# Kernel tuning notes

Measured on AMD Instinct MI355X. Metric: run time of the kernel, lower is better.

Reference implementation:

```python
import jax, jax.numpy as jnp
import numpy as np

S, B, H = 4096, 1, 2048       # [seq, batch, hidden] layout (NeoX convention)
NP, HN = 16, H // 16          # heads, head dim
ROT = int(HN * 0.25)          # rotary_ndims = 32 (rotary_pct=0.25)
ROPE_BASE = 10000.0


def setup_inputs() -> dict:
    key = jax.random.key(0)
    k0, k1, k2 = jax.random.split(key, 3)
    hidden_states = jax.random.normal(k0, (S, B, H), jnp.float32) * 0.02
    # causal left-to-right mask: True = masked out (filled with -10000)
    attention_mask = jnp.triu(jnp.ones((1, 1, S, S), bool), k=1)
    w_qkv = jax.random.normal(k1, (3 * H, H), jnp.float32) * (1.0 / np.sqrt(H))
    w_dense = jax.random.normal(k2, (H, H), jnp.float32) * (1.0 / np.sqrt(H))
    b_dense = jnp.zeros((H,), jnp.float32)
    return {"hidden_states": hidden_states, "attention_mask": attention_mask,
            "w_qkv": w_qkv, "w_dense": w_dense, "b_dense": b_dense}


def _apply_rope(x, pos):
    # x: [s, b, np, ROT]; NeoX rotate_half convention
    inv_freq = 1.0 / (ROPE_BASE ** (jnp.arange(0, ROT, 2, dtype=jnp.float32) / ROT))
    freqs = pos[:, None] * inv_freq[None, :]              # [s, ROT/2]
    emb = jnp.concatenate([freqs, freqs], axis=-1)        # [s, ROT]
    cos = jnp.cos(emb)[:, None, None, :]
    sin = jnp.sin(emb)[:, None, None, :]
    x1, x2 = jnp.split(x, 2, axis=-1)
    rot = jnp.concatenate([-x2, x1], axis=-1)
    return x * cos + rot * sin


def reference(hidden_states, attention_mask, w_qkv, w_dense, b_dense):
    s, b, h = hidden_states.shape
    # fused QKV projection (no bias), reshape to [s, b, np, 3*hn], split
    qkv = (hidden_states @ w_qkv.T).reshape(s, b, NP, 3 * HN)
    q, k, v = jnp.split(qkv, 3, axis=-1)                  # each [s, b, np, hn]
    # partial rotary embedding on first ROT dims
    pos = jnp.arange(s, dtype=jnp.float32)
    q = jnp.concatenate([_apply_rope(q[..., :ROT], pos), q[..., ROT:]], axis=-1)
    k = jnp.concatenate([_apply_rope(k[..., :ROT], pos), k[..., ROT:]], axis=-1)
    # raw attention scores [b, np, s_q, s_k], scale 1/sqrt(hn)
    scores = jnp.einsum('sbhd,tbhd->bhst', q, k) / np.float32(np.sqrt(HN))
    # ltor mask: fill masked positions with -10000, softmax in fp32
    scores = jnp.where(attention_mask, jnp.float32(-10000.0), scores)
    probs = jax.nn.softmax(scores.astype(jnp.float32), axis=-1).astype(hidden_states.dtype)
    # context [s, b, np, hn] -> [s, b, h]
    ctx = jnp.einsum('bhst,tbhd->sbhd', probs, v).reshape(s, b, h)
    return ctx @ w_dense.T + b_dense
```

## Files before the change

### kernel.cpp

```cpp
#include <hip/hip_runtime.h>

#define S_LEN 4096
#define HID   2048
#define NHEAD 16
#define HDIM  128
#define QSCALE_L2E 0.12751664352f

typedef float  f32x4  __attribute__((ext_vector_type(4)));
typedef float  f32x16 __attribute__((ext_vector_type(16)));
typedef __bf16 bf16x8 __attribute__((ext_vector_type(8)));
typedef unsigned u32x4 __attribute__((ext_vector_type(4)));
typedef unsigned u32x2 __attribute__((ext_vector_type(2)));

#define MFMA16(a, b, c) __builtin_amdgcn_mfma_f32_16x16x32_bf16((a), (b), (c), 0, 0, 0)
#define MFMA32(a, b, c) __builtin_amdgcn_mfma_f32_32x32x16_bf16((a), (b), (c), 0, 0, 0)

__device__ __forceinline__ void gld16(const void* g, void* l) {
  __builtin_amdgcn_global_load_lds(
      (const __attribute__((address_space(1))) void*)(unsigned long long)(g),
      (__attribute__((address_space(3))) void*)(unsigned long long)(l),
      16, 0, 0);
}

__device__ __forceinline__ unsigned short f2bf(float f) {
  union { float f; unsigned u; } v; v.f = f;
  unsigned r = v.u + 0x7FFFu + ((v.u >> 16) & 1u);
  return (unsigned short)(r >> 16);
}
__device__ __forceinline__ float bf2f(unsigned short h) {
  union { unsigned u; float f; } v; v.u = ((unsigned)h) << 16;
  return v.f;
}
__device__ __forceinline__ unsigned cvtpk_bf16(float a, float b) {
  unsigned r;
  asm("v_cvt_pk_bf16_f32 %0, %1, %2" : "=v"(r) : "v"(a), "v"(b));
  return r;
}
__device__ __forceinline__ u32x2 pls(unsigned a, unsigned b) {
  return __builtin_amdgcn_permlane32_swap(a, b, false, false);
}
__device__ __forceinline__ float asf(unsigned u) { return __builtin_bit_cast(float, u); }
__device__ __forceinline__ unsigned asu(float f) { return __builtin_bit_cast(unsigned, f); }

__global__ __launch_bounds__(256) void cvt3_kernel(
    const float* __restrict__ s0, const float* __restrict__ s1,
    const float* __restrict__ s2, unsigned short* __restrict__ d0,
    unsigned short* __restrict__ d1, unsigned short* __restrict__ d2) {
  int i = (blockIdx.x * 256 + threadIdx.x) * 4;
  const float* src; unsigned short* dst;
  if (i < 8388608) { src = s0; dst = d0; }
  else if (i < 20971520) { src = s1 - 8388608; dst = d1 - 8388608; }
  else { src = s2 - 20971520; dst = d2 - 20971520; }
  const float4 v = *(const float4*)(src + i);
  ushort4 o;
  o.x = f2bf(v.x); o.y = f2bf(v.y); o.z = f2bf(v.z); o.w = f2bf(v.w);
  *(ushort4*)(dst + i) = o;
}

template <int EPI>
__global__ __launch_bounds__(512, 2) void gemm256_kernel(
    const unsigned short* __restrict__ A, const unsigned short* __restrict__ B,
    unsigned short* __restrict__ Qb, unsigned short* __restrict__ Kb,
    unsigned short* __restrict__ Vt,
    const float* __restrict__ bias, float* __restrict__ out) {
  __shared__ __align__(16) unsigned char sm[147456];
  constexpr int K = HID;
  constexpr int NT = K / 64;
  const int b = (int)blockIdx.x;
  const int bm = (b & 7) * 2 + ((b >> 3) & 1);
  const int bn = b >> 4;
  const int row0 = bm * 256, col0 = bn * 128;
  const int tid = threadIdx.x;
  const int wid = tid >> 6, lane = tid & 63;
  const int g = lane >> 4, r16 = lane & 15;
  const int wm = wid >> 1, wn = wid & 1;

  auto stageA = [&](int t, int bufo) {
    const int k0 = t * 64;
#pragma unroll
    for (int h = 0; h < 2; ++h)
#pragma unroll
      for (int cc = 0; cc < 2; ++cc) {
        const int chunk = cc * 512 + tid;
        const int r = chunk >> 3, c7 = chunk & 7;
        gld16(A + (row0 + h * 128 + r) * K + k0 + ((c7 ^ (r & 7)) << 3),
              sm + bufo + h * 16384 + chunk * 16);
      }
  };
  auto stageB = [&](int t, int bufo) {
    const int k0 = t * 64;
#pragma unroll
    for (int cc = 0; cc < 2; ++cc) {
      const int chunk = cc * 512 + tid;
      const int r = chunk >> 3, c7 = chunk & 7;
      gld16(B + (col0 + r) * K + k0 + ((c7 ^ (r & 7)) << 3),
            sm + bufo + 32768 + chunk * 16);
    }
  };

  f32x4 acc[4][4] = {};

  int aoff[4], boff[4];
#pragma unroll
  for (int m = 0; m < 4; ++m) {
    const int r = (wm & 1) * 64 + m * 16 + r16;
    aoff[m] = (wm >> 1) * 16384 + r * 128 + ((g * 16) ^ ((r & 7) << 4));
  }
#pragma unroll
  for (int n = 0; n < 4; ++n) {
    const int r = wn * 64 + n * 16 + r16;
    boff[n] = 32768 + r * 128 + ((g * 16) ^ ((r & 7) << 4));
  }

  stageA(0, 0); stageB(0, 0);
  stageA(1, 49152); stageB(1, 49152);
  asm volatile("s_waitcnt vmcnt(6)" ::: "memory");
  __builtin_amdgcn_s_barrier();
  __builtin_amdgcn_sched_barrier(0);

  int curo = 0, stgo = 98304;
  for (int t = 0; t < NT; ++t) {
    const bool st = (t + 2 < NT);
    bf16x8 af[4], bfv[4];
#pragma unroll
    for (int m = 0; m < 4; ++m) af[m] = *(const bf16x8*)(sm + curo + aoff[m]);
#pragma unroll
    for (int n = 0; n < 4; ++n) bfv[n] = *(const bf16x8*)(sm + curo + boff[n]);
    if (st) stageA(t + 2, stgo);
    __builtin_amdgcn_s_setprio(1);
#pragma unroll
    for (int m = 0; m < 4; ++m)
#pragma unroll
      for (int n = 0; n < 4; ++n) acc[m][n] = MFMA16(af[m], bfv[n], acc[m][n]);
    __builtin_amdgcn_s_setprio(0);
#pragma unroll
    for (int m = 0; m < 4; ++m) af[m] = *(const bf16x8*)(sm + curo + (aoff[m] ^ 64));
#pragma unroll
    for (int n = 0; n < 4; ++n) bfv[n] = *(const bf16x8*)(sm + curo + (boff[n] ^ 64));
    if (st) stageB(t + 2, stgo);
    __builtin_amdgcn_s_setprio(1);
#pragma unroll
    for (int m = 0; m < 4; ++m)
#pragma unroll
      for (int n = 0; n < 4; ++n) acc[m][n] = MFMA16(af[m], bfv[n], acc[m][n]);
    __builtin_amdgcn_s_setprio(0);
    if (st) asm volatile("s_waitcnt vmcnt(6)" ::: "memory");
    else    asm volatile("s_waitcnt vmcnt(0)" ::: "memory");
    __builtin_amdgcn_s_barrier();
    __builtin_amdgcn_sched_barrier(0);
    curo = (curo == 98304) ? 0 : curo + 49152;
    stgo = (stgo == 98304) ? 0 : stgo + 49152;
  }

  if constexpr (EPI == 0) {
    const int type = bn % 3, p = bn / 3;
    if (type <= 1) {
      unsigned short* Ob = (type == 0) ? Qb : Kb;
      const float qs = (type == 0) ? QSCALE_L2E : 1.0f;
      const float invf = exp2f(-(float)r16 * 0.8304820237218406f);
#pragma unroll
      for (int m = 0; m < 4; ++m) {
        const int s0 = row0 + wm * 64 + m * 16 + g * 4;
        if (wn == 0) {
#pragma unroll
          for (int r = 0; r < 4; ++r) {
            const float ang = (float)(s0 + r) * invf;
            const float c = cosf(ang), sn = sinf(ang);
            const float x = acc[m][0][r] * qs, y = acc[m][1][r] * qs;
            unsigned short* dst = Ob + (p * S_LEN + s0 + r) * HDIM;
            dst[r16]      = f2bf(x * c - y * sn);
            dst[16 + r16] = f2bf(y * c + x * sn);
          }
#pragma unroll
          for (int n = 2; n < 4; ++n)
#pragma unroll
            for (int r = 0; r < 4; ++r)
              Ob[(p * S_LEN + s0 + r) * HDIM + n * 16 + r16] = f2bf(acc[m][n][r] * qs);
        } else {
#pragma unroll
          for (int n = 0; n < 4; ++n)
#pragma unroll
            for (int r = 0; r < 4; ++r)
              Ob[(p * S_LEN + s0 + r) * HDIM + 64 + n * 16 + r16] = f2bf(acc[m][n][r] * qs);
        }
      }
    } else {
#pragma unroll
      for (int m = 0; m < 4; ++m) {
        const int s0 = row0 + wm * 64 + m * 16 + g * 4;
#pragma unroll
        for (int n = 0; n < 4; ++n) {
          const int d = wn * 64 + n * 16 + r16;
          ushort4 o;
          o.x = f2bf(acc[m][n][0]); o.y = f2bf(acc[m][n][1]);
          o.z = f2bf(acc[m][n][2]); o.w = f2bf(acc[m][n][3]);
          *(ushort4*)(Vt + (p * HDIM + d) * S_LEN + s0) = o;
        }
      }
    }
  } else {
#pragma unroll
    for (int m = 0; m < 4; ++m) {
      const int s0 = row0 + wm * 64 + m * 16 + g * 4;
#pragma unroll
      for (int n = 0; n < 4; ++n) {
        const int col = col0 + wn * 64 + n * 16 + r16;
        const float bv = bias[col];
#pragma unroll
        for (int r = 0; r < 4; ++r)
          out[(s0 + r) * HID + col] = acc[m][n][r] + bv;
      }
    }
  }
}

__global__ __launch_bounds__(256, 2) void attn_kernel(
    const unsigned short* __restrict__ Qb, const unsigned short* __restrict__ Kb,
    const unsigned short* __restrict__ Vt, unsigned short* __restrict__ Ctx) {
  __shared__ __align__(16) unsigned char sm[81920];
  const int b = (int)blockIdx.x;
  const int p = b & 15;
  const int qt = (b < 256) ? (b >> 4) : 47 - (b >> 4);
  const int tid = threadIdx.x, wid = tid >> 6, lane = tid & 63;
  const int l31 = lane & 31, hi = lane >> 5;
  const int xr = (l31 & 7) << 4;

  const int q0w = qt * 128 + wid * 32;
  const int qg = q0w + l31;
  const int nt = 2 * (qt + 1);
  const int np = nt >> 1;

  auto stage = [&](int t, int ko, int vo) {
    const unsigned short* kb = Kb + (p * S_LEN + t * 64) * HDIM;
    const unsigned short* vb = Vt + p * HDIM * S_LEN + t * 64;
#pragma unroll
    for (int c = 0; c < 4; ++c) {
      const int chunk = c * 256 + tid;
      const int byteoff = chunk * 16;
      const int j = byteoff >> 8, cbK = (byteoff >> 4) & 15;
      gld16(kb + j * HDIM + ((cbK ^ (j & 7)) << 3), sm + ko + chunk * 16);
      const int dd = byteoff >> 7, cbV = (byteoff >> 4) & 7;
      gld16(vb + dd * S_LEN + ((cbV ^ (dd & 7)) << 3), sm + vo + chunk * 16);
    }
  };

  bf16x8 qf[8];
  f32x16 acc[4] = {};
  float m_s = -1e30f, l_s = 0.f;

  auto qk = [&](f32x16& s0, f32x16& s1, const unsigned char* kl) {
    __builtin_amdgcn_s_setprio(1);
#pragma unroll
    for (int dd = 0; dd < 8; ++dd) {
      bf16x8 k0 = *(const bf16x8*)(kl + l31 * 256 + (((dd * 2 + hi) << 4) ^ xr));
      bf16x8 k1 = *(const bf16x8*)(kl + (32 + l31) * 256 + (((dd * 2 + hi) << 4) ^ xr));
      s0 = MFMA32(k0, qf[dd], s0);
      s1 = MFMA32(k1, qf[dd], s1);
    }
    __builtin_amdgcn_s_setprio(0);
  };

  auto smpv = [&](f32x16& s0, f32x16& s1, int t, int vo) {
    const unsigned char* vl = sm + vo;
    if (t * 64 + 63 > q0w) {
#pragma unroll
      for (int r = 0; r < 16; ++r) {
        const int kv0 = t * 64 + ((r & 3) + 8 * (r >> 2)) + 4 * hi;
        if (kv0 > qg) s0[r] = -1e30f;
        if (kv0 + 32 > qg) s1[r] = -1e30f;
      }
    }
    float mx[16];
#pragma unroll
    for (int r = 0; r < 16; ++r) mx[r] = fmaxf(s0[r], s1[r]);
#pragma unroll
    for (int r = 0; r < 8; ++r) mx[r] = fmaxf(mx[r], mx[r + 8]);
#pragma unroll
    for (int r = 0; r < 4; ++r) mx[r] = fmaxf(mx[r], mx[r + 4]);
    mx[0] = fmaxf(fmaxf(mx[0], mx[2]), fmaxf(mx[1], mx[3]));
    float pm;
    {
      u32x2 e = pls(asu(mx[0]), asu(mx[0]));
      pm = fmaxf(asf(e.x), asf(e.y));
    }
    if (__any(pm > m_s + 11.5f)) {
      const float mn = fmaxf(m_s, pm);
      const float scl = exp2f(m_s - mn);
#pragma unroll
      for (int d32 = 0; d32 < 4; ++d32)
#pragma unroll
        for (int r = 0; r < 16; ++r) acc[d32][r] *= scl;
      l_s *= scl;
      m_s = mn;
    }
#pragma unroll
    for (int r = 0; r < 16; ++r) {
      s0[r] = exp2f(s0[r] - m_s);
      s1[r] = exp2f(s1[r] - m_s);
    }
    bf16x8 pf[4];
#define PACKB(B, SV, base)                                                        \
    {                                                                             \
      unsigned X0 = cvtpk_bf16(SV[base + 0], SV[base + 1]);                       \
      unsigned X1 = cvtpk_bf16(SV[base + 2], SV[base + 3]);                       \
      unsigned Y0 = cvtpk_bf16(SV[base + 4], SV[base + 5]);                       \
      unsigned Y1 = cvtpk_bf16(SV[base + 6], SV[base + 7]);                       \
      u32x2 e0 = pls(X0, Y0);                                                     \
      u32x2 e1 = pls(X1, Y1);                                                     \
      u32x4 pw;                                                                   \
      pw.x = e0.x; pw.y = e1.x; pw.z = e0.y; pw.w = e1.y;                         \
      pf[B] = __builtin_bit_cast(bf16x8, pw);                                     \
    }
    PACKB(0, s0, 0)
    PACKB(1, s0, 8)
    PACKB(2, s1, 0)
    PACKB(3, s1, 8)
#undef PACKB
    __builtin_amdgcn_s_setprio(1);
#pragma unroll
    for (int d32 = 0; d32 < 4; ++d32) {
#pragma unroll
      for (int bb = 0; bb < 4; ++bb) {
        bf16x8 vf = *(const bf16x8*)(vl + (d32 * 32 + l31) * 128 + (((bb * 2 + hi) << 4) ^ xr));
        acc[d32] = MFMA32(vf, pf[bb], acc[d32]);
      }
    }
    __builtin_amdgcn_s_setprio(0);
    float s_[8];
#pragma unroll
    for (int r = 0; r < 8; ++r) s_[r] = (s0[r] + s0[r + 8]) + (s1[r] + s1[r + 8]);
#pragma unroll
    for (int r = 0; r < 4; ++r) s_[r] += s_[r + 4];
    const float rs = (s_[0] + s_[1]) + (s_[2] + s_[3]);
    u32x2 e = pls(asu(rs), asu(rs));
    l_s += asf(e.x) + asf(e.y);
  };

  {
    const unsigned short* qp_ = Qb + (p * S_LEN + qg) * HDIM + hi * 8;
#pragma unroll
    for (int dd = 0; dd < 8; ++dd) qf[dd] = *(const bf16x8*)(qp_ + dd * 16);
  }
  stage(0, 0, 32768);
  stage(1, 16384, 49152);
  int vcur = 32768, vnext = 49152, vstage = 65536;
  __syncthreads();
  f32x16 sA0 = {}, sA1 = {};
  qk(sA0, sA1, sm);
  __syncthreads();

  for (int tt = 0; tt < np; ++tt) {
    const bool more = (tt + 1 < np);
    const int t = 2 * tt;
    f32x16 sB0 = {}, sB1 = {};
    qk(sB0, sB1, sm + 16384);
    if (more) stage(t + 2, 0, vstage);
    smpv(sA0, sA1, t, vcur);
    { int tmp = vcur; vcur = vnext; vnext = vstage; vstage = tmp; }
    __syncthreads();
    if (more) {
      sA0 = {}; sA1 = {};
      qk(sA0, sA1, sm);
      stage(t + 3, 16384, vstage);
    }
    smpv(sB0, sB1, t + 1, vcur);
    { int tmp = vcur; vcur = vnext; vnext = vstage; vstage = tmp; }
    __syncthreads();
  }

  const float inv = 1.0f / l_s;
  unsigned short* cbase = Ctx + qg * HID + p * HDIM;
#pragma unroll
  for (int d32 = 0; d32 < 4; ++d32)
#pragma unroll
    for (int r = 0; r < 16; ++r) {
      const int d = d32 * 32 + ((r & 3) + 8 * (r >> 2)) + 4 * hi;
      cbase[d] = f2bf(acc[d32][r] * inv);
    }
}

extern "C" void kernel_launch(void* const* d_in, const int* in_sizes, int n_in,
                              void* d_out, int out_size, void* d_ws, size_t ws_size,
                              hipStream_t stream) {
  (void)in_sizes; (void)n_in; (void)out_size; (void)ws_size;
  const float* hidden = (const float*)d_in[0];
  const float* wqkv   = (const float*)d_in[2];
  const float* wdense = (const float*)d_in[3];
  const float* bdense = (const float*)d_in[4];
  float* out = (float*)d_out;

  char* ws = (char*)d_ws;
  unsigned short* hiddenB = (unsigned short*)(ws);
  unsigned short* wqkvB   = (unsigned short*)(ws + 16777216);
  unsigned short* wdenseB = (unsigned short*)(ws + 41943040);
  unsigned short* Qb      = (unsigned short*)(ws + 50331648);
  unsigned short* Kb      = (unsigned short*)(ws + 67108864);
  unsigned short* Vt      = (unsigned short*)(ws + 83886080);
  unsigned short* ctxB    = (unsigned short*)(ws + 100663296);

  cvt3_kernel<<<24576, 256, 0, stream>>>(hidden, wqkv, wdense, hiddenB, wqkvB, wdenseB);
  gemm256_kernel<0><<<768, 512, 0, stream>>>(hiddenB, wqkvB, Qb, Kb, Vt, nullptr, nullptr);
  attn_kernel<<<512, 256, 0, stream>>>(Qb, Kb, Vt, ctxB);
  gemm256_kernel<1><<<256, 512, 0, stream>>>(ctxB, wdenseB, nullptr, nullptr, nullptr, bdense, out);
}
```

Baseline: 301.3 us.

## Split long causal query tiles across two blocks and merge partials

The attention grid grows from 512 to 768 blocks. The 16 longest query tiles per head now have their KV range split in two halves, each processed by its own block, which writes unnormalized bf16 partial outputs plus per-row (max, sum). A new merge kernel combines the two halves with log-sum-exp rescaling into the context buffer. The goal is to shorten the critical path set by the longest causal tiles and balance work across CUs. The cost is an extra launch, extra global traffic for the partials, and reuse of workspace (the hiddenB and wqkvB region) that the QKV GEMM has already finished with.

```diff
diff --git a/kernel.cpp b/kernel.cpp
--- a/kernel.cpp
+++ b/kernel.cpp
@@ -216,19 +216,30 @@
 
 __global__ __launch_bounds__(256, 2) void attn_kernel(
     const unsigned short* __restrict__ Qb, const unsigned short* __restrict__ Kb,
-    const unsigned short* __restrict__ Vt, unsigned short* __restrict__ Ctx) {
+    const unsigned short* __restrict__ Vt, unsigned short* __restrict__ Ctx,
+    unsigned short* __restrict__ Opart, float2* __restrict__ MLpart) {
   __shared__ __align__(16) unsigned char sm[81920];
   const int b = (int)blockIdx.x;
   const int p = b & 15;
-  const int qt = (b < 256) ? (b >> 4) : 47 - (b >> 4);
+  const int piece = b >> 4;
+  int qt, t0, ntp, split, half;
+  if (piece < 32) {
+    qt = 31 - (piece >> 1);
+    half = piece & 1;
+    const int hA = (qt + 2) & ~1;
+    if (half == 0) { t0 = 0; ntp = hA; }
+    else { t0 = hA; ntp = 2 * (qt + 1) - hA; }
+    split = 1;
+  } else {
+    qt = 47 - piece; t0 = 0; ntp = 2 * (qt + 1); split = 0; half = 0;
+  }
   const int tid = threadIdx.x, wid = tid >> 6, lane = tid & 63;
   const int l31 = lane & 31, hi = lane >> 5;
   const int xr = (l31 & 7) << 4;
 
   const int q0w = qt * 128 + wid * 32;
   const int qg = q0w + l31;
-  const int nt = 2 * (qt + 1);
-  const int np = nt >> 1;
+  const int np = ntp >> 1;
 
   auto stage = [&](int t, int ko, int vo) {
     const unsigned short* kb = Kb + (p * S_LEN + t * 64) * HDIM;
@@ -341,8 +352,8 @@
 #pragma unroll
     for (int dd = 0; dd < 8; ++dd) qf[dd] = *(const bf16x8*)(qp_ + dd * 16);
   }
-  stage(0, 0, 32768);
-  stage(1, 16384, 49152);
+  stage(t0, 0, 32768);
+  stage(t0 + 1, 16384, 49152);
   int vcur = 32768, vnext = 49152, vstage = 65536;
   __syncthreads();
   f32x16 sA0 = {}, sA1 = {};
@@ -351,7 +362,7 @@
 
   for (int tt = 0; tt < np; ++tt) {
     const bool more = (tt + 1 < np);
-    const int t = 2 * tt;
+    const int t = t0 + 2 * tt;
     f32x16 sB0 = {}, sB1 = {};
     qk(sB0, sB1, sm + 16384);
     if (more) stage(t + 2, 0, vstage);
@@ -368,15 +379,49 @@
     __syncthreads();
   }
 
-  const float inv = 1.0f / l_s;
-  unsigned short* cbase = Ctx + qg * HID + p * HDIM;
-#pragma unroll
-  for (int d32 = 0; d32 < 4; ++d32)
-#pragma unroll
-    for (int r = 0; r < 16; ++r) {
-      const int d = d32 * 32 + ((r & 3) + 8 * (r >> 2)) + 4 * hi;
-      cbase[d] = f2bf(acc[d32][r] * inv);
-    }
+  if (!split) {
+    const float inv = 1.0f / l_s;
+    unsigned short* cbase = Ctx + qg * HID + p * HDIM;
+#pragma unroll
+    for (int d32 = 0; d32 < 4; ++d32)
+#pragma unroll
+      for (int r = 0; r < 16; ++r) {
+        const int d = d32 * 32 + ((r & 3) + 8 * (r >> 2)) + 4 * hi;
+        cbase[d] = f2bf(acc[d32][r] * inv);
+      }
+  } else {
+    const int pidx = ((p * 16 + (qt - 16)) * 2 + half);
+    const int row = wid * 32 + l31;
+    unsigned short* ob = Opart + pidx * 16384 + row * 128;
+#pragma unroll
+    for (int d32 = 0; d32 < 4; ++d32)
+#pragma unroll
+      for (int r = 0; r < 16; ++r) {
+        const int d = d32 * 32 + ((r & 3) + 8 * (r >> 2)) + 4 * hi;
+        ob[d] = f2bf(acc[d32][r]);
+      }
+    if (hi == 0) MLpart[pidx * 128 + row] = make_float2(m_s, l_s);
+  }
+}
+
+__global__ __launch_bounds__(256) void merge_kernel(
+    const unsigned short* __restrict__ Opart, const float2* __restrict__ MLpart,
+    unsigned short* __restrict__ Ctx) {
+  const int rid = blockIdx.x * 2 + (threadIdx.x >> 7);
+  const int d = threadIdx.x & 127;
+  const int head = rid >> 11;
+  const int sqt = (rid >> 7) & 15;
+  const int row = rid & 127;
+  const int qt = 16 + sqt;
+  const int pA = (head * 16 + sqt) * 2;
+  const float2 mlA = MLpart[pA * 128 + row];
+  const float2 mlB = MLpart[(pA + 1) * 128 + row];
+  const float m = fmaxf(mlA.x, mlB.x);
+  const float wA = exp2f(mlA.x - m), wB = exp2f(mlB.x - m);
+  const float linv = 1.0f / (mlA.y * wA + mlB.y * wB);
+  const float oA = bf2f(Opart[pA * 16384 + row * 128 + d]);
+  const float oB = bf2f(Opart[(pA + 1) * 16384 + row * 128 + d]);
+  Ctx[(qt * 128 + row) * HID + head * HDIM + d] = f2bf((oA * wA + oB * wB) * linv);
 }
 
 extern "C" void kernel_launch(void* const* d_in, const int* in_sizes, int n_in,
@@ -397,9 +442,12 @@
   unsigned short* Kb      = (unsigned short*)(ws + 67108864);
   unsigned short* Vt      = (unsigned short*)(ws + 83886080);
   unsigned short* ctxB    = (unsigned short*)(ws + 100663296);
+  unsigned short* Opart   = (unsigned short*)(ws);
+  float2*         MLpart  = (float2*)(ws + 33554432);
 
   cvt3_kernel<<<24576, 256, 0, stream>>>(hidden, wqkv, wdense, hiddenB, wqkvB, wdenseB);
   gemm256_kernel<0><<<768, 512, 0, stream>>>(hiddenB, wqkvB, Qb, Kb, Vt, nullptr, nullptr);
-  attn_kernel<<<512, 256, 0, stream>>>(Qb, Kb, Vt, ctxB);
+  attn_kernel<<<768, 256, 0, stream>>>(Qb, Kb, Vt, ctxB, Opart, MLpart);
+  merge_kernel<<<16384, 256, 0, stream>>>(Opart, MLpart, ctxB);
   gemm256_kernel<1><<<256, 512, 0, stream>>>(ctxB, wdenseB, nullptr, nullptr, nullptr, bdense, out);
 }
```

Measured after the change: 312.7 us. 1.04x slower.

## Load V fragments directly from global into registers, shrink LDS to K only

Applied to the files above, without the earlier changes.

The attention kernel no longer stages the transposed V tiles through LDS. Each lane now loads its V fragments straight from global memory into 16 registers before the QK step that precedes their use, which cuts LDS from 80 KB to 32 KB and removes the triple-buffer rotation. The aim is to lower LDS footprint and traffic. In exchange it adds register pressure, with 16 more bf16x8 values live, and exposes uncoalesced strided global-load latency right before the PV MFMAs.

```diff
diff --git a/kernel.cpp b/kernel.cpp
--- a/kernel.cpp
+++ b/kernel.cpp
@@ -217,7 +217,7 @@
 __global__ __launch_bounds__(256, 2) void attn_kernel(
     const unsigned short* __restrict__ Qb, const unsigned short* __restrict__ Kb,
     const unsigned short* __restrict__ Vt, unsigned short* __restrict__ Ctx) {
-  __shared__ __align__(16) unsigned char sm[81920];
+  __shared__ __align__(16) unsigned char sm[32768];
   const int b = (int)blockIdx.x;
   const int p = b & 15;
   const int qt = (b < 256) ? (b >> 4) : 47 - (b >> 4);
@@ -230,23 +230,31 @@
   const int nt = 2 * (qt + 1);
   const int np = nt >> 1;
 
-  auto stage = [&](int t, int ko, int vo) {
+  const unsigned short* vb = Vt + p * HDIM * S_LEN;
+
+  auto stageK = [&](int t, int ko) {
     const unsigned short* kb = Kb + (p * S_LEN + t * 64) * HDIM;
-    const unsigned short* vb = Vt + p * HDIM * S_LEN + t * 64;
 #pragma unroll
     for (int c = 0; c < 4; ++c) {
       const int chunk = c * 256 + tid;
-      const int byteoff = chunk * 16;
-      const int j = byteoff >> 8, cbK = (byteoff >> 4) & 15;
+      const int j = chunk >> 4, cbK = chunk & 15;
       gld16(kb + j * HDIM + ((cbK ^ (j & 7)) << 3), sm + ko + chunk * 16);
-      const int dd = byteoff >> 7, cbV = (byteoff >> 4) & 7;
-      gld16(vb + dd * S_LEN + ((cbV ^ (dd & 7)) << 3), sm + vo + chunk * 16);
     }
   };
 
   bf16x8 qf[8];
+  bf16x8 vf[16];
   f32x16 acc[4] = {};
   float m_s = -1e30f, l_s = 0.f;
+
+  auto loadV = [&](int t) {
+#pragma unroll
+    for (int d32 = 0; d32 < 4; ++d32)
+#pragma unroll
+      for (int bb = 0; bb < 4; ++bb)
+        vf[d32 * 4 + bb] = *(const bf16x8*)(
+            vb + (d32 * 32 + l31) * S_LEN + t * 64 + (bb * 2 + hi) * 8);
+  };
 
   auto qk = [&](f32x16& s0, f32x16& s1, const unsigned char* kl) {
     __builtin_amdgcn_s_setprio(1);
@@ -260,8 +268,7 @@
     __builtin_amdgcn_s_setprio(0);
   };
 
-  auto smpv = [&](f32x16& s0, f32x16& s1, int t, int vo) {
-    const unsigned char* vl = sm + vo;
+  auto smpv = [&](f32x16& s0, f32x16& s1, int t) {
     if (t * 64 + 63 > q0w) {
 #pragma unroll
       for (int r = 0; r < 16; ++r) {
@@ -320,10 +327,8 @@
 #pragma unroll
     for (int d32 = 0; d32 < 4; ++d32) {
 #pragma unroll
-      for (int bb = 0; bb < 4; ++bb) {
-        bf16x8 vf = *(const bf16x8*)(vl + (d32 * 32 + l31) * 128 + (((bb * 2 + hi) << 4) ^ xr));
-        acc[d32] = MFMA32(vf, pf[bb], acc[d32]);
-      }
+      for (int bb = 0; bb < 4; ++bb)
+        acc[d32] = MFMA32(vf[d32 * 4 + bb], pf[bb], acc[d32]);
     }
     __builtin_amdgcn_s_setprio(0);
     float s_[8];
@@ -341,9 +346,8 @@
 #pragma unroll
     for (int dd = 0; dd < 8; ++dd) qf[dd] = *(const bf16x8*)(qp_ + dd * 16);
   }
-  stage(0, 0, 32768);
-  stage(1, 16384, 49152);
-  int vcur = 32768, vnext = 49152, vstage = 65536;
+  stageK(0, 0);
+  stageK(1, 16384);
   __syncthreads();
   f32x16 sA0 = {}, sA1 = {};
   qk(sA0, sA1, sm);
@@ -352,19 +356,19 @@
   for (int tt = 0; tt < np; ++tt) {
     const bool more = (tt + 1 < np);
     const int t = 2 * tt;
+    loadV(t);
     f32x16 sB0 = {}, sB1 = {};
     qk(sB0, sB1, sm + 16384);
-    if (more) stage(t + 2, 0, vstage);
-    smpv(sA0, sA1, t, vcur);
-    { int tmp = vcur; vcur = vnext; vnext = vstage; vstage = tmp; }
+    if (more) stageK(t + 2, 0);
+    smpv(sA0, sA1, t);
     __syncthreads();
+    loadV(t + 1);
     if (more) {
       sA0 = {}; sA1 = {};
       qk(sA0, sA1, sm);
-      stage(t + 3, 16384, vstage);
-    }
-    smpv(sB0, sB1, t + 1, vcur);
-    { int tmp = vcur; vcur = vnext; vnext = vstage; vstage = tmp; }
+      stageK(t + 3, 16384);
+    }
+    smpv(sB0, sB1, t + 1);
     __syncthreads();
   }
 
```

New measurement: 519.7 us. 1.72x slower.

## Split KV range across two wave groups per attention block and merge partials

Applied to the files above, without the earlier changes.

The attention block grows from 256 to 512 threads. The two 4-wave groups process disjoint halves of the causal KV range with 32-key tiles, and each keeps its own running max, sum and output. At the end the partial results are merged through shared memory. This raises the number of waves working on each query tile and shortens the serial KV loop. In exchange it adds a merge step, a final barrier and more register pressure under launch_bounds(512,2), and each tile now does half as many MFMAs per softmax step.

```diff
diff --git a/kernel.cpp b/kernel.cpp
--- a/kernel.cpp
+++ b/kernel.cpp
@@ -214,7 +214,7 @@
   }
 }
 
-__global__ __launch_bounds__(256, 2) void attn_kernel(
+__global__ __launch_bounds__(512, 2) void attn_kernel(
     const unsigned short* __restrict__ Qb, const unsigned short* __restrict__ Kb,
     const unsigned short* __restrict__ Vt, unsigned short* __restrict__ Ctx) {
   __shared__ __align__(16) unsigned char sm[81920];
@@ -222,25 +222,33 @@
   const int p = b & 15;
   const int qt = (b < 256) ? (b >> 4) : 47 - (b >> 4);
   const int tid = threadIdx.x, wid = tid >> 6, lane = tid & 63;
+  const int g = wid >> 2, wv = wid & 3, gtid = tid & 255;
   const int l31 = lane & 31, hi = lane >> 5;
   const int xr = (l31 & 7) << 4;
-
-  const int q0w = qt * 128 + wid * 32;
+  const int GB = g * 40960;
+
+  const int q0w = qt * 128 + wv * 32;
   const int qg = q0w + l31;
-  const int nt = 2 * (qt + 1);
-  const int np = nt >> 1;
-
-  auto stage = [&](int t, int ko, int vo) {
-    const unsigned short* kb = Kb + (p * S_LEN + t * 64) * HDIM;
-    const unsigned short* vb = Vt + p * HDIM * S_LEN + t * 64;
-#pragma unroll
-    for (int c = 0; c < 4; ++c) {
-      const int chunk = c * 256 + tid;
-      const int byteoff = chunk * 16;
-      const int j = byteoff >> 8, cbK = (byteoff >> 4) & 15;
-      gld16(kb + j * HDIM + ((cbK ^ (j & 7)) << 3), sm + ko + chunk * 16);
-      const int dd = byteoff >> 7, cbV = (byteoff >> 4) & 7;
-      gld16(vb + dd * S_LEN + ((cbV ^ (dd & 7)) << 3), sm + vo + chunk * 16);
+  const int Th = 2 * (qt + 1);
+  const int np = qt + 1;
+  const int tg0 = g * Th;
+
+  auto stageK = [&](int tg, int ko) {
+    const unsigned short* kb = Kb + (p * S_LEN + tg * 32) * HDIM;
+#pragma unroll
+    for (int c = 0; c < 2; ++c) {
+      const int chunk = c * 256 + gtid;
+      const int j = chunk >> 4, cb = chunk & 15;
+      gld16(kb + j * HDIM + ((cb ^ (j & 7)) << 3), sm + ko + chunk * 16);
+    }
+  };
+  auto stageV = [&](int tg, int vo) {
+    const unsigned short* vbase = Vt + p * HDIM * S_LEN + tg * 32;
+#pragma unroll
+    for (int c = 0; c < 2; ++c) {
+      const int chunk = c * 256 + gtid;
+      const int d = chunk >> 2, cb = chunk & 3;
+      gld16(vbase + d * S_LEN + ((cb ^ (d & 3)) << 3), sm + vo + chunk * 16);
     }
   };
 
@@ -248,33 +256,28 @@
   f32x16 acc[4] = {};
   float m_s = -1e30f, l_s = 0.f;
 
-  auto qk = [&](f32x16& s0, f32x16& s1, const unsigned char* kl) {
+  auto qk = [&](f32x16& s, const unsigned char* kl) {
     __builtin_amdgcn_s_setprio(1);
 #pragma unroll
     for (int dd = 0; dd < 8; ++dd) {
       bf16x8 k0 = *(const bf16x8*)(kl + l31 * 256 + (((dd * 2 + hi) << 4) ^ xr));
-      bf16x8 k1 = *(const bf16x8*)(kl + (32 + l31) * 256 + (((dd * 2 + hi) << 4) ^ xr));
-      s0 = MFMA32(k0, qf[dd], s0);
-      s1 = MFMA32(k1, qf[dd], s1);
+      s = MFMA32(k0, qf[dd], s);
     }
     __builtin_amdgcn_s_setprio(0);
   };
 
-  auto smpv = [&](f32x16& s0, f32x16& s1, int t, int vo) {
+  auto smpv = [&](f32x16& s, int tg, int vo) {
     const unsigned char* vl = sm + vo;
-    if (t * 64 + 63 > q0w) {
+    if (tg * 32 + 31 > q0w) {
 #pragma unroll
       for (int r = 0; r < 16; ++r) {
-        const int kv0 = t * 64 + ((r & 3) + 8 * (r >> 2)) + 4 * hi;
-        if (kv0 > qg) s0[r] = -1e30f;
-        if (kv0 + 32 > qg) s1[r] = -1e30f;
-      }
-    }
-    float mx[16];
-#pragma unroll
-    for (int r = 0; r < 16; ++r) mx[r] = fmaxf(s0[r], s1[r]);
-#pragma unroll
-    for (int r = 0; r < 8; ++r) mx[r] = fmaxf(mx[r], mx[r + 8]);
+        const int kv0 = tg * 32 + ((r & 3) + 8 * (r >> 2)) + 4 * hi;
+        if (kv0 > qg) s[r] = -1e30f;
+      }
+    }
+    float mx[8];
+#pragma unroll
+    for (int r = 0; r < 8; ++r) mx[r] = fmaxf(s[r], s[r + 8]);
 #pragma unroll
     for (int r = 0; r < 4; ++r) mx[r] = fmaxf(mx[r], mx[r + 4]);
     mx[0] = fmaxf(fmaxf(mx[0], mx[2]), fmaxf(mx[1], mx[3]));
@@ -294,11 +297,8 @@
       m_s = mn;
     }
 #pragma unroll
-    for (int r = 0; r < 16; ++r) {
-      s0[r] = exp2f(s0[r] - m_s);
-      s1[r] = exp2f(s1[r] - m_s);
-    }
-    bf16x8 pf[4];
+    for (int r = 0; r < 16; ++r) s[r] = exp2f(s[r] - m_s);
+    bf16x8 pf[2];
 #define PACKB(B, SV, base)                                                        \
     {                                                                             \
       unsigned X0 = cvtpk_bf16(SV[base + 0], SV[base + 1]);                       \
@@ -311,24 +311,23 @@
       pw.x = e0.x; pw.y = e1.x; pw.z = e0.y; pw.w = e1.y;                         \
       pf[B] = __builtin_bit_cast(bf16x8, pw);                                     \
     }
-    PACKB(0, s0, 0)
-    PACKB(1, s0, 8)
-    PACKB(2, s1, 0)
-    PACKB(3, s1, 8)
+    PACKB(0, s, 0)
+    PACKB(1, s, 8)
 #undef PACKB
     __builtin_amdgcn_s_setprio(1);
 #pragma unroll
     for (int d32 = 0; d32 < 4; ++d32) {
-#pragma unroll
-      for (int bb = 0; bb < 4; ++bb) {
-        bf16x8 vf = *(const bf16x8*)(vl + (d32 * 32 + l31) * 128 + (((bb * 2 + hi) << 4) ^ xr));
+      const int d = d32 * 32 + l31;
+#pragma unroll
+      for (int bb = 0; bb < 2; ++bb) {
+        bf16x8 vf = *(const bf16x8*)(vl + d * 64 + ((((bb * 2 + hi) << 4)) ^ ((l31 & 3) << 4)));
         acc[d32] = MFMA32(vf, pf[bb], acc[d32]);
       }
     }
     __builtin_amdgcn_s_setprio(0);
     float s_[8];
 #pragma unroll
-    for (int r = 0; r < 8; ++r) s_[r] = (s0[r] + s0[r + 8]) + (s1[r] + s1[r + 8]);
+    for (int r = 0; r < 8; ++r) s_[r] = s[r] + s[r + 8];
 #pragma unroll
     for (int r = 0; r < 4; ++r) s_[r] += s_[r + 4];
     const float rs = (s_[0] + s_[1]) + (s_[2] + s_[3]);
@@ -341,42 +340,70 @@
 #pragma unroll
     for (int dd = 0; dd < 8; ++dd) qf[dd] = *(const bf16x8*)(qp_ + dd * 16);
   }
-  stage(0, 0, 32768);
-  stage(1, 16384, 49152);
-  int vcur = 32768, vnext = 49152, vstage = 65536;
+  stageK(tg0, GB);
+  stageV(tg0, GB + 16384);
+  stageK(tg0 + 1, GB + 8192);
+  stageV(tg0 + 1, GB + 24576);
+  int vcur = GB + 16384, vnext = GB + 24576, vstage = GB + 32768;
   __syncthreads();
-  f32x16 sA0 = {}, sA1 = {};
-  qk(sA0, sA1, sm);
+  f32x16 sA = {};
+  qk(sA, sm + GB);
   __syncthreads();
 
   for (int tt = 0; tt < np; ++tt) {
     const bool more = (tt + 1 < np);
-    const int t = 2 * tt;
-    f32x16 sB0 = {}, sB1 = {};
-    qk(sB0, sB1, sm + 16384);
-    if (more) stage(t + 2, 0, vstage);
-    smpv(sA0, sA1, t, vcur);
+    const int t = tg0 + 2 * tt;
+    f32x16 sB = {};
+    qk(sB, sm + GB + 8192);
+    if (more) { stageK(t + 2, GB); stageV(t + 2, vstage); }
+    smpv(sA, t, vcur);
     { int tmp = vcur; vcur = vnext; vnext = vstage; vstage = tmp; }
     __syncthreads();
     if (more) {
-      sA0 = {}; sA1 = {};
-      qk(sA0, sA1, sm);
-      stage(t + 3, 16384, vstage);
-    }
-    smpv(sB0, sB1, t + 1, vcur);
+      sA = {};
+      qk(sA, sm + GB);
+      stageK(t + 3, GB + 8192);
+      stageV(t + 3, vstage);
+    }
+    smpv(sB, t + 1, vcur);
     { int tmp = vcur; vcur = vnext; vnext = vstage; vstage = tmp; }
     __syncthreads();
   }
 
-  const float inv = 1.0f / l_s;
-  unsigned short* cbase = Ctx + qg * HID + p * HDIM;
-#pragma unroll
-  for (int d32 = 0; d32 < 4; ++d32)
-#pragma unroll
-    for (int r = 0; r < 16; ++r) {
-      const int d = d32 * 32 + ((r & 3) + 8 * (r >> 2)) + 4 * hi;
-      cbase[d] = f2bf(acc[d32][r] * inv);
-    }
+  if (g == 1) {
+    const int base = wv * 16384;
+#pragma unroll
+    for (int d32 = 0; d32 < 4; ++d32)
+#pragma unroll
+      for (int k = 0; k < 4; ++k) {
+        float4 v4;
+        v4.x = acc[d32][k * 4 + 0]; v4.y = acc[d32][k * 4 + 1];
+        v4.z = acc[d32][k * 4 + 2]; v4.w = acc[d32][k * 4 + 3];
+        *(float4*)(sm + base + d32 * 4096 + k * 1024 + lane * 16) = v4;
+      }
+    if (hi == 0)
+      *(float2*)(sm + 65536 + (wv * 32 + l31) * 8) = make_float2(m_s, l_s);
+  }
+  __syncthreads();
+  if (g == 0) {
+    const float2 ml1 = *(const float2*)(sm + 65536 + (wv * 32 + l31) * 8);
+    const float mm = fmaxf(m_s, ml1.x);
+    const float w0 = exp2f(m_s - mm), w1 = exp2f(ml1.x - mm);
+    const float linv = 1.0f / (l_s * w0 + ml1.y * w1);
+    unsigned short* cbase = Ctx + qg * HID + p * HDIM;
+#pragma unroll
+    for (int d32 = 0; d32 < 4; ++d32)
+#pragma unroll
+      for (int k = 0; k < 4; ++k) {
+        const float4 o1 = *(const float4*)(sm + wv * 16384 + d32 * 4096 + k * 1024 + lane * 16);
+        const float ov[4] = {o1.x, o1.y, o1.z, o1.w};
+#pragma unroll
+        for (int j = 0; j < 4; ++j) {
+          const int d = d32 * 32 + j + 8 * k + 4 * hi;
+          cbase[d] = f2bf((acc[d32][k * 4 + j] * w0 + ov[j] * w1) * linv);
+        }
+      }
+  }
 }
 
 extern "C" void kernel_launch(void* const* d_in, const int* in_sizes, int n_in,
@@ -400,6 +427,6 @@
 
   cvt3_kernel<<<24576, 256, 0, stream>>>(hidden, wqkv, wdense, hiddenB, wqkvB, wdenseB);
   gemm256_kernel<0><<<768, 512, 0, stream>>>(hiddenB, wqkvB, Qb, Kb, Vt, nullptr, nullptr);
-  attn_kernel<<<512, 256, 0, stream>>>(Qb, Kb, Vt, ctxB);
+  attn_kernel<<<512, 512, 0, stream>>>(Qb, Kb, Vt, ctxB);
   gemm256_kernel<1><<<256, 512, 0, stream>>>(ctxB, wdenseB, nullptr, nullptr, nullptr, bdense, out);
 }
```

Measured after the change: 282.2 us. 1.07x faster.
